# Optimization experiments

Measured on AMD Instinct MI355X. Metric: run time of the kernel, lower is better.

## Reference

```python
import jax, jax.numpy as jnp
import numpy as np
import math

NUM_HEADS = 12
EMBED_DIM = 768

def setup_inputs() -> dict:
    key = jax.random.key(0)
    ks = jax.random.split(key, 9)
    B, T, D = 2, 2048, EMBED_DIM
    s = 1.0 / math.sqrt(D)
    inp = {
        "x": jax.random.normal(ks[0], (B, T, D), dtype=jnp.float32),
        "Wq": jax.random.normal(ks[1], (D, D), dtype=jnp.float32) * s,
        "bq": jnp.zeros((D,), dtype=jnp.float32),
        "Wk": jax.random.normal(ks[2], (D, D), dtype=jnp.float32) * s,
        "bk": jnp.zeros((D,), dtype=jnp.float32),
        "Wv": jax.random.normal(ks[3], (D, D), dtype=jnp.float32) * s,
        "bv": jnp.zeros((D,), dtype=jnp.float32),
        "Wo": jax.random.normal(ks[4], (D, D), dtype=jnp.float32) * s,
        "bo": jnp.zeros((D,), dtype=jnp.float32),
    }
    return inp

def reference(x, Wq, bq, Wk, bk, Wv, bv, Wo, bo):
    B, T, D = x.shape
    H = NUM_HEADS
    Dh = D // H
    # QKV projections, split heads: [B, H, T, Dh]
    def proj(W, b):
        y = x @ W.T + b
        return y.reshape(B, T, H, Dh).transpose(0, 2, 1, 3)
    q = proj(Wq, bq)
    k = proj(Wk, bk)
    v = proj(Wv, bv)
    scores = jnp.einsum('bhtd,bhsd->bhts', q, k) / math.sqrt(Dh)  # [B,H,T,T]
    attn = jax.nn.softmax(scores, axis=-1)
    ctx = jnp.einsum('bhts,bhsd->bhtd', attn, v)  # [B,H,T,Dh]
    ctx = ctx.transpose(0, 2, 1, 3).reshape(B, T, D)
    out = ctx @ Wo.T + bo
    return out
```

## Files before the change

kernel.cpp:

```cpp
#include <hip/hip_runtime.h>
#include <math.h>

using f32x4   = __attribute__((ext_vector_type(4))) float;
using bf16x8  = __attribute__((ext_vector_type(8))) short;

constexpr int Bb = 2;
constexpr int T  = 2048;
constexpr int D  = 768;
constexpr int H  = 12;
constexpr int Dh = 64;
constexpr int M  = Bb * T;
constexpr int NQKV = 3 * D;
#define SCALE_Q 0.18033688011112042f

__device__ __forceinline__ unsigned short f2bf(float f) {
    unsigned u = __float_as_uint(f);
    u += 0x7fffu + ((u >> 16) & 1u);
    return (unsigned short)(u >> 16);
}

__device__ __forceinline__ ushort4 f2bf4(float4 f) {
    return make_ushort4(f2bf(f.x), f2bf(f.y), f2bf(f.z), f2bf(f.w));
}

__device__ __forceinline__ unsigned permpk(float hi_f, float lo_f) {
    return __builtin_amdgcn_perm(__float_as_uint(hi_f), __float_as_uint(lo_f),
                                 0x07060302u);
}

__device__ __forceinline__ void async_copy16(const void* g, void* lds_base) {
    __builtin_amdgcn_global_load_lds(
        (const __attribute__((address_space(1))) unsigned int*)g,
        (__attribute__((address_space(3))) unsigned int*)lds_base, 16, 0, 0);
}

__global__ __launch_bounds__(256) void prep_kernel(
    const float4* __restrict__ x,
    const float4* __restrict__ Wq, const float4* __restrict__ Wk,
    const float4* __restrict__ Wv, const float4* __restrict__ Wo,
    const float* __restrict__ bq, const float* __restrict__ bk, const float* __restrict__ bv,
    ushort4* __restrict__ Xb, ushort4* __restrict__ Wqkvb, ushort4* __restrict__ Wob,
    float* __restrict__ biasS)
{
    const int stride = gridDim.x * 256;
    const int i0 = blockIdx.x * 256 + threadIdx.x;
    const int NX = M * D / 4;
    const int NW = D * D / 4;
    for (int i = i0; i < NX; i += stride) Xb[i] = f2bf4(x[i]);
    for (int i = i0; i < NW; i += stride) {
        Wqkvb[i]          = f2bf4(Wq[i]);
        Wqkvb[NW + i]     = f2bf4(Wk[i]);
        Wqkvb[2 * NW + i] = f2bf4(Wv[i]);
        Wob[i]            = f2bf4(Wo[i]);
    }
    for (int i = i0; i < D; i += stride) {
        biasS[i]         = bq[i];
        biasS[D + i]     = bk[i];
        biasS[2 * D + i] = bv[i];
    }
}

template <int MODE, int TM>
__global__ __launch_bounds__(256) void gemm_bt_kernel(
    const unsigned short* __restrict__ A, const unsigned short* __restrict__ Bm,
    const float* __restrict__ bias, const int Kdim, const int Ndim,
    float* __restrict__ Cout,
    unsigned short* __restrict__ Qo, unsigned short* __restrict__ Ko,
    unsigned short* __restrict__ Vo)
{
    constexpr int IW  = TM / 32;
    constexpr int NCH = (TM + 128) / 8;
    __shared__ unsigned short Sm[(TM + 128) * 64];
    const int tid  = threadIdx.x;
    const int lane = tid & 63, wv = tid >> 6;
    const int l15  = lane & 15, l4 = lane >> 4;
    const int wr   = wv >> 1,  wc = wv & 1;

    const int lin = blockIdx.y * gridDim.x + blockIdx.x;
    const int gx  = (lin >> 3) % gridDim.x;
    const int gy  = (lin / (8 * gridDim.x)) * 8 + (lin & 7);
    const int row0 = gy * TM, col0 = gx * 128;

    f32x4 acc[IW][4];
    #pragma unroll
    for (int i = 0; i < IW; ++i)
        #pragma unroll
        for (int j = 0; j < 4; ++j)
            acc[i][j] = (f32x4){0.f, 0.f, 0.f, 0.f};

    for (int k0 = 0; k0 < Kdim; k0 += 64) {
        __syncthreads();
        #pragma unroll
        for (int ch0 = 0; ch0 < NCH; ch0 += 4) {
            const int ch = ch0 + wv;
            const int offb = ch * 1024;
            const int off  = offb + lane * 16;
            const int r  = off >> 7;
            const int bl = (off & 127) >> 4;
            const int gc = (bl ^ (r & 7)) << 3;
            const unsigned short* src = (r < TM)
                ? A  + (size_t)(row0 + r) * Kdim + k0 + gc
                : Bm + (size_t)(col0 + (r - TM)) * Kdim + k0 + gc;
            async_copy16(src, (char*)Sm + offb);
        }
        __syncthreads();

        #pragma unroll
        for (int c = 0; c < 2; ++c) {
            bf16x8 af[IW], bfr[4];
            #pragma unroll
            for (int i = 0; i < IW; ++i) {
                const int row = wr * (TM / 2) + i * 16 + l15;
                af[i] = *(const bf16x8*)((const char*)Sm +
                        row * 128 + (((c << 2) + l4) ^ (row & 7)) * 16);
            }
            #pragma unroll
            for (int j = 0; j < 4; ++j) {
                const int row = TM + wc * 64 + j * 16 + l15;
                bfr[j] = *(const bf16x8*)((const char*)Sm +
                        row * 128 + (((c << 2) + l4) ^ (row & 7)) * 16);
            }
            #pragma unroll
            for (int i = 0; i < IW; ++i)
                #pragma unroll
                for (int j = 0; j < 4; ++j)
                    acc[i][j] = __builtin_amdgcn_mfma_f32_16x16x32_bf16(af[i], bfr[j], acc[i][j], 0, 0, 0);
        }
    }

    if (MODE == 0) {
        #pragma unroll
        for (int j = 0; j < 4; ++j) {
            const int n = col0 + wc * 64 + j * 16 + l15;
            const float bv_ = bias[n];
            #pragma unroll
            for (int i = 0; i < IW; ++i) {
                #pragma unroll
                for (int r = 0; r < 4; ++r) {
                    const int m = row0 + wr * (TM / 2) + i * 16 + l4 * 4 + r;
                    Cout[(size_t)m * Ndim + n] = acc[i][j][r] + bv_;
                }
            }
        }
    } else {
        #pragma unroll
        for (int j = 0; j < 4; ++j) {
            const int n = col0 + wc * 64 + j * 16 + l15;
            const int which = n / D;
            const int hd = n % D;
            const int h = hd >> 6, d = hd & 63;
            const float bv_ = bias[n];
            if (which == 2) {
                #pragma unroll
                for (int i = 0; i < IW; ++i) {
                    const int m0 = row0 + wr * (TM / 2) + i * 16 + l4 * 4;
                    const int b = m0 >> 11, t = m0 & (T - 1);
                    const int g = (t >> 2) & 3, h16 = (t >> 4) & 1;
                    const int tp = (t & ~31) | (g << 3) | (h16 << 2);
                    float4 v4;
                    v4.x = acc[i][j][0] + bv_; v4.y = acc[i][j][1] + bv_;
                    v4.z = acc[i][j][2] + bv_; v4.w = acc[i][j][3] + bv_;
                    *(ushort4*)&Vo[((size_t)(b * H + h) * Dh + d) * T + tp] = f2bf4(v4);
                }
            } else {
                const float scale = (which == 0) ? SCALE_Q : 1.0f;
                unsigned short* dst = (which == 0) ? Qo : Ko;
                #pragma unroll
                for (int i = 0; i < IW; ++i) {
                    #pragma unroll
                    for (int r = 0; r < 4; ++r) {
                        const int m = row0 + wr * (TM / 2) + i * 16 + l4 * 4 + r;
                        const int b = m >> 11, t = m & (T - 1);
                        dst[((size_t)(b * H + h) * T + t) * Dh + d] =
                            f2bf((acc[i][j][r] + bv_) * scale);
                    }
                }
            }
        }
    }
}

__global__ __launch_bounds__(256) void attn_kernel(
    const unsigned short* __restrict__ Q, const unsigned short* __restrict__ Kg,
    const unsigned short* __restrict__ Vt, unsigned short* __restrict__ Ctx)
{
    __shared__ unsigned short Ks[2][64 * 64];
    __shared__ unsigned short Vs[2][64 * 64];
    const int bh = blockIdx.y;
    const int q0 = blockIdx.x * 128;
    const int tid = threadIdx.x, lane = tid & 63, wv = tid >> 6;
    const int l15 = lane & 15, l4 = lane >> 4;
    const unsigned short* Qp = Q  + (size_t)bh * T * Dh;
    const unsigned short* Kp = Kg + (size_t)bh * T * Dh;
    const unsigned short* Vp = Vt + (size_t)bh * Dh * T;

    bf16x8 qf[2][2];
    #pragma unroll
    for (int qg = 0; qg < 2; ++qg)
        #pragma unroll
        for (int c = 0; c < 2; ++c)
            qf[qg][c] = *(const bf16x8*)&Qp[(size_t)(q0 + wv * 32 + qg * 16 + l15) * Dh + c * 32 + l4 * 8];

    const short oneb = (short)0x3F80;
    const bf16x8 onesf = {oneb, oneb, oneb, oneb, oneb, oneb, oneb, oneb};

    auto load_tiles = [&](int kt, int buf) {
        #pragma unroll
        for (int i = 0; i < 2; ++i) {
            const int offb = wv * 2048 + i * 1024;
            const int off  = offb + lane * 16;
            const int r = off >> 7;
            const int blk = (off & 127) >> 4;
            const int gc = (blk ^ (r & 7)) << 3;
            async_copy16(Kp + (size_t)(kt + r) * Dh + gc, (char*)&Ks[buf][0] + offb);
            async_copy16(Vp + (size_t)r * T + kt + gc,    (char*)&Vs[buf][0] + offb);
        }
    };

    load_tiles(0, 0);
    f32x4 o[2][4], oL[2];
    #pragma unroll
    for (int qg = 0; qg < 2; ++qg) {
        #pragma unroll
        for (int nj = 0; nj < 4; ++nj) o[qg][nj] = (f32x4){0.f, 0.f, 0.f, 0.f};
        oL[qg] = (f32x4){0.f, 0.f, 0.f, 0.f};
    }

    for (int kt64 = 0; kt64 < T / 64; ++kt64) {
        const int cur = kt64 & 1;
        __syncthreads();
        if (kt64 + 1 < T / 64) load_tiles((kt64 + 1) * 64, cur ^ 1);

        const char* Kb = (const char*)&Ks[cur][0];
        const char* Vb = (const char*)&Vs[cur][0];

        f32x4 Sa[2][2];
        #pragma unroll
        for (int t = 0; t < 2; ++t)
            #pragma unroll
            for (int qg = 0; qg < 2; ++qg)
                Sa[t][qg] = (f32x4){0.f, 0.f, 0.f, 0.f};
        #pragma unroll
        for (int c = 0; c < 2; ++c) {
            #pragma unroll
            for (int t = 0; t < 2; ++t) {
                const int row = t * 16 + l15;
                bf16x8 kb = *(const bf16x8*)(Kb + row * 128 + (((c << 2) + l4) ^ (row & 7)) * 16);
                #pragma unroll
                for (int qg = 0; qg < 2; ++qg)
                    Sa[t][qg] = __builtin_amdgcn_mfma_f32_16x16x32_bf16(kb, qf[qg][c], Sa[t][qg], 0, 0, 0);
            }
        }
        #pragma unroll
        for (int t = 0; t < 2; ++t)
            #pragma unroll
            for (int qg = 0; qg < 2; ++qg)
                #pragma unroll
                for (int r = 0; r < 4; ++r)
                    Sa[t][qg][r] = __builtin_amdgcn_exp2f(Sa[t][qg][r]);
        union { unsigned u[4]; bf16x8 v; } p0[2];
        #pragma unroll
        for (int qg = 0; qg < 2; ++qg) {
            p0[qg].u[0] = permpk(Sa[0][qg][1], Sa[0][qg][0]);
            p0[qg].u[1] = permpk(Sa[0][qg][3], Sa[0][qg][2]);
            p0[qg].u[2] = permpk(Sa[1][qg][1], Sa[1][qg][0]);
            p0[qg].u[3] = permpk(Sa[1][qg][3], Sa[1][qg][2]);
        }

        f32x4 Sb[2][2];
        #pragma unroll
        for (int t = 0; t < 2; ++t)
            #pragma unroll
            for (int qg = 0; qg < 2; ++qg)
                Sb[t][qg] = (f32x4){0.f, 0.f, 0.f, 0.f};
        #pragma unroll
        for (int c = 0; c < 2; ++c) {
            #pragma unroll
            for (int t = 0; t < 2; ++t) {
                const int row = (t + 2) * 16 + l15;
                bf16x8 kb = *(const bf16x8*)(Kb + row * 128 + (((c << 2) + l4) ^ (row & 7)) * 16);
                #pragma unroll
                for (int qg = 0; qg < 2; ++qg)
                    Sb[t][qg] = __builtin_amdgcn_mfma_f32_16x16x32_bf16(kb, qf[qg][c], Sb[t][qg], 0, 0, 0);
            }
        }

        #pragma unroll
        for (int qg = 0; qg < 2; ++qg)
            oL[qg] = __builtin_amdgcn_mfma_f32_16x16x32_bf16(p0[qg].v, onesf, oL[qg], 0, 0, 0);
        #pragma unroll
        for (int nj = 0; nj < 4; ++nj) {
            const int row = nj * 16 + l15;
            bf16x8 vb = *(const bf16x8*)(Vb + row * 128 + ((l4) ^ (row & 7)) * 16);
            #pragma unroll
            for (int qg = 0; qg < 2; ++qg)
                o[qg][nj] = __builtin_amdgcn_mfma_f32_16x16x32_bf16(p0[qg].v, vb, o[qg][nj], 0, 0, 0);
        }

        #pragma unroll
        for (int t = 0; t < 2; ++t)
            #pragma unroll
            for (int qg = 0; qg < 2; ++qg)
                #pragma unroll
                for (int r = 0; r < 4; ++r)
                    Sb[t][qg][r] = __builtin_amdgcn_exp2f(Sb[t][qg][r]);
        union { unsigned u[4]; bf16x8 v; } p1[2];
        #pragma unroll
        for (int qg = 0; qg < 2; ++qg) {
            p1[qg].u[0] = permpk(Sb[0][qg][1], Sb[0][qg][0]);
            p1[qg].u[1] = permpk(Sb[0][qg][3], Sb[0][qg][2]);
            p1[qg].u[2] = permpk(Sb[1][qg][1], Sb[1][qg][0]);
            p1[qg].u[3] = permpk(Sb[1][qg][3], Sb[1][qg][2]);
        }

        #pragma unroll
        for (int qg = 0; qg < 2; ++qg)
            oL[qg] = __builtin_amdgcn_mfma_f32_16x16x32_bf16(p1[qg].v, onesf, oL[qg], 0, 0, 0);
        #pragma unroll
        for (int nj = 0; nj < 4; ++nj) {
            const int row = nj * 16 + l15;
            bf16x8 vb = *(const bf16x8*)(Vb + row * 128 + ((4 + l4) ^ (row & 7)) * 16);
            #pragma unroll
            for (int qg = 0; qg < 2; ++qg)
                o[qg][nj] = __builtin_amdgcn_mfma_f32_16x16x32_bf16(p1[qg].v, vb, o[qg][nj], 0, 0, 0);
        }
    }

    const int b = bh / H, h = bh % H;
    #pragma unroll
    for (int qg = 0; qg < 2; ++qg) {
        #pragma unroll
        for (int r = 0; r < 4; ++r) {
            const float inv = 1.0f / oL[qg][r];
            const int t = q0 + wv * 32 + qg * 16 + l4 * 4 + r;
            #pragma unroll
            for (int nj = 0; nj < 4; ++nj) {
                const int col = h * 64 + nj * 16 + l15;
                Ctx[(size_t)(b * T + t) * D + col] = f2bf(o[qg][nj][r] * inv);
            }
        }
    }
}

extern "C" void kernel_launch(void* const* d_in, const int* in_sizes, int n_in,
                              void* d_out, int out_size, void* d_ws, size_t ws_size,
                              hipStream_t stream) {
    const float* x  = (const float*)d_in[0];
    const float* Wq = (const float*)d_in[1];
    const float* bq = (const float*)d_in[2];
    const float* Wk = (const float*)d_in[3];
    const float* bk = (const float*)d_in[4];
    const float* Wv = (const float*)d_in[5];
    const float* bv = (const float*)d_in[6];
    const float* Wo = (const float*)d_in[7];
    const float* bo = (const float*)d_in[8];
    float* out = (float*)d_out;

    char* w = (char*)d_ws;
    auto alloc = [&](size_t bytes) {
        char* p = w; w += (bytes + 255) & ~(size_t)255; return p;
    };
    unsigned short* Xb    = (unsigned short*)alloc((size_t)M * D * 2);
    unsigned short* Wqkvb = (unsigned short*)alloc((size_t)NQKV * D * 2);
    unsigned short* Wob   = (unsigned short*)alloc((size_t)D * D * 2);
    float*          biasS = (float*)alloc((size_t)NQKV * 4);
    unsigned short* Qb    = (unsigned short*)alloc((size_t)M * D * 2);
    unsigned short* Kb    = (unsigned short*)alloc((size_t)M * D * 2);
    unsigned short* Vtb   = (unsigned short*)alloc((size_t)M * D * 2);
    unsigned short* Ctxb  = (unsigned short*)alloc((size_t)M * D * 2);

    prep_kernel<<<1024, 256, 0, stream>>>(
        (const float4*)x, (const float4*)Wq, (const float4*)Wk, (const float4*)Wv,
        (const float4*)Wo, bq, bk, bv,
        (ushort4*)Xb, (ushort4*)Wqkvb, (ushort4*)Wob, biasS);

    gemm_bt_kernel<1, 128><<<dim3(NQKV / 128, M / 128), 256, 0, stream>>>(
        Xb, Wqkvb, biasS, D, NQKV, nullptr, Qb, Kb, Vtb);

    attn_kernel<<<dim3(T / 128, Bb * H), 256, 0, stream>>>(Qb, Kb, Vtb, Ctxb);

    gemm_bt_kernel<0, 64><<<dim3(D / 128, M / 64), 256, 0, stream>>>(
        Ctxb, Wob, bo, D, D, out, nullptr, nullptr, nullptr);
}
```

Before: 168.5 us.

## Split attention KV range across two blocks and double-buffer output-projection GEMM

The attention kernel now processes only half of the key/value sequence per block, with a new grid z-dimension selecting the half. It writes unnormalized fp32 partial outputs and row sums, and a new combine kernel adds the halves, normalizes, and writes bf16 context. The intent is to double the attention grid so the blocks spread more evenly across compute units. The out-projection GEMM gains an optional double-buffered LDS pipeline and uses a smaller 32-row tile, and the prep kernel launches more blocks. The cost is extra global traffic for the fp32 partials plus one more kernel launch. Summing the halves is only correct because the softmax uses no per-block running max.

```diff
diff --git a/kernel.cpp b/kernel.cpp
--- a/kernel.cpp
+++ b/kernel.cpp
@@ -11,6 +11,7 @@
 constexpr int Dh = 64;
 constexpr int M  = Bb * T;
 constexpr int NQKV = 3 * D;
+constexpr int NBH = Bb * H;
 #define SCALE_Q 0.18033688011112042f
 
 __device__ __forceinline__ unsigned short f2bf(float f) {
@@ -60,7 +61,7 @@
     }
 }
 
-template <int MODE, int TM>
+template <int MODE, int TM, int DB>
 __global__ __launch_bounds__(256) void gemm_bt_kernel(
     const unsigned short* __restrict__ A, const unsigned short* __restrict__ Bm,
     const float* __restrict__ bias, const int Kdim, const int Ndim,
@@ -70,7 +71,8 @@
 {
     constexpr int IW  = TM / 32;
     constexpr int NCH = (TM + 128) / 8;
-    __shared__ unsigned short Sm[(TM + 128) * 64];
+    constexpr int TB  = (TM + 128) * 128;
+    __shared__ unsigned short Sm[(TM + 128) * 64 * (DB ? 2 : 1)];
     const int tid  = threadIdx.x;
     const int lane = tid & 63, wv = tid >> 6;
     const int l15  = lane & 15, l4 = lane >> 4;
@@ -81,15 +83,7 @@
     const int gy  = (lin / (8 * gridDim.x)) * 8 + (lin & 7);
     const int row0 = gy * TM, col0 = gx * 128;
 
-    f32x4 acc[IW][4];
-    #pragma unroll
-    for (int i = 0; i < IW; ++i)
-        #pragma unroll
-        for (int j = 0; j < 4; ++j)
-            acc[i][j] = (f32x4){0.f, 0.f, 0.f, 0.f};
-
-    for (int k0 = 0; k0 < Kdim; k0 += 64) {
-        __syncthreads();
+    auto stage = [&](int k0, int b) {
         #pragma unroll
         for (int ch0 = 0; ch0 < NCH; ch0 += 4) {
             const int ch = ch0 + wv;
@@ -101,9 +95,29 @@
             const unsigned short* src = (r < TM)
                 ? A  + (size_t)(row0 + r) * Kdim + k0 + gc
                 : Bm + (size_t)(col0 + (r - TM)) * Kdim + k0 + gc;
-            async_copy16(src, (char*)Sm + offb);
-        }
+            async_copy16(src, (char*)Sm + b * TB + offb);
+        }
+    };
+
+    f32x4 acc[IW][4];
+    #pragma unroll
+    for (int i = 0; i < IW; ++i)
+        #pragma unroll
+        for (int j = 0; j < 4; ++j)
+            acc[i][j] = (f32x4){0.f, 0.f, 0.f, 0.f};
+
+    if (DB) stage(0, 0);
+
+    for (int k0 = 0, it = 0; k0 < Kdim; k0 += 64, ++it) {
+        const int cur = DB ? (it & 1) : 0;
         __syncthreads();
+        if (DB) {
+            if (k0 + 64 < Kdim) stage(k0 + 64, cur ^ 1);
+        } else {
+            stage(k0, 0);
+            __syncthreads();
+        }
+        const char* Sb_ = (const char*)Sm + cur * TB;
 
         #pragma unroll
         for (int c = 0; c < 2; ++c) {
@@ -111,13 +125,13 @@
             #pragma unroll
             for (int i = 0; i < IW; ++i) {
                 const int row = wr * (TM / 2) + i * 16 + l15;
-                af[i] = *(const bf16x8*)((const char*)Sm +
+                af[i] = *(const bf16x8*)(Sb_ +
                         row * 128 + (((c << 2) + l4) ^ (row & 7)) * 16);
             }
             #pragma unroll
             for (int j = 0; j < 4; ++j) {
                 const int row = TM + wc * 64 + j * 16 + l15;
-                bfr[j] = *(const bf16x8*)((const char*)Sm +
+                bfr[j] = *(const bf16x8*)(Sb_ +
                         row * 128 + (((c << 2) + l4) ^ (row & 7)) * 16);
             }
             #pragma unroll
@@ -182,11 +196,13 @@
 
 __global__ __launch_bounds__(256) void attn_kernel(
     const unsigned short* __restrict__ Q, const unsigned short* __restrict__ Kg,
-    const unsigned short* __restrict__ Vt, unsigned short* __restrict__ Ctx)
+    const unsigned short* __restrict__ Vt,
+    float* __restrict__ Po, float* __restrict__ PoL)
 {
     __shared__ unsigned short Ks[2][64 * 64];
     __shared__ unsigned short Vs[2][64 * 64];
     const int bh = blockIdx.y;
+    const int half = blockIdx.z;
     const int q0 = blockIdx.x * 128;
     const int tid = threadIdx.x, lane = tid & 63, wv = tid >> 6;
     const int l15 = lane & 15, l4 = lane >> 4;
@@ -217,7 +233,9 @@
         }
     };
 
-    load_tiles(0, 0);
+    const int NT = T / 128;
+    const int kt0 = half * NT;
+    load_tiles(kt0 * 64, 0);
     f32x4 o[2][4], oL[2];
     #pragma unroll
     for (int qg = 0; qg < 2; ++qg) {
@@ -226,10 +244,11 @@
         oL[qg] = (f32x4){0.f, 0.f, 0.f, 0.f};
     }
 
-    for (int kt64 = 0; kt64 < T / 64; ++kt64) {
-        const int cur = kt64 & 1;
+    for (int it = 0; it < NT; ++it) {
+        const int kt64 = kt0 + it;
+        const int cur = it & 1;
         __syncthreads();
-        if (kt64 + 1 < T / 64) load_tiles((kt64 + 1) * 64, cur ^ 1);
+        if (it + 1 < NT) load_tiles((kt64 + 1) * 64, cur ^ 1);
 
         const char* Kb = (const char*)&Ks[cur][0];
         const char* Vb = (const char*)&Vs[cur][0];
@@ -326,20 +345,36 @@
         }
     }
 
-    const int b = bh / H, h = bh % H;
+    const size_t base = (size_t)(half * NBH + bh) * T;
     #pragma unroll
     for (int qg = 0; qg < 2; ++qg) {
         #pragma unroll
         for (int r = 0; r < 4; ++r) {
-            const float inv = 1.0f / oL[qg][r];
             const int t = q0 + wv * 32 + qg * 16 + l4 * 4 + r;
             #pragma unroll
-            for (int nj = 0; nj < 4; ++nj) {
-                const int col = h * 64 + nj * 16 + l15;
-                Ctx[(size_t)(b * T + t) * D + col] = f2bf(o[qg][nj][r] * inv);
-            }
-        }
-    }
+            for (int nj = 0; nj < 4; ++nj)
+                Po[(base + t) * 64 + nj * 16 + l15] = o[qg][nj][r];
+            if (l15 == 0) PoL[base + t] = oL[qg][r];
+        }
+    }
+}
+
+__global__ __launch_bounds__(256) void combine_kernel(
+    const float4* __restrict__ Po, const float* __restrict__ PoL,
+    unsigned short* __restrict__ Ctx)
+{
+    const int idx = blockIdx.x * 256 + threadIdx.x;
+    const int d4 = idx & 15;
+    const int rem = idx >> 4;
+    const int t = rem & (T - 1), bh = rem >> 11;
+    const float4 a = Po[(size_t)rem * 16 + d4];
+    const float4 c = Po[(size_t)NBH * T * 16 + (size_t)rem * 16 + d4];
+    const float inv = 1.0f / (PoL[rem] + PoL[NBH * T + rem]);
+    const int b = bh / H, h = bh % H;
+    float4 v;
+    v.x = (a.x + c.x) * inv; v.y = (a.y + c.y) * inv;
+    v.z = (a.z + c.z) * inv; v.w = (a.w + c.w) * inv;
+    *(ushort4*)&Ctx[(size_t)(b * T + t) * D + h * 64 + d4 * 4] = f2bf4(v);
 }
 
 extern "C" void kernel_launch(void* const* d_in, const int* in_sizes, int n_in,
@@ -368,17 +403,22 @@
     unsigned short* Kb    = (unsigned short*)alloc((size_t)M * D * 2);
     unsigned short* Vtb   = (unsigned short*)alloc((size_t)M * D * 2);
     unsigned short* Ctxb  = (unsigned short*)alloc((size_t)M * D * 2);
-
-    prep_kernel<<<1024, 256, 0, stream>>>(
+    float*          Po    = (float*)alloc((size_t)2 * NBH * T * 64 * 4);
+    float*          PoL   = (float*)alloc((size_t)2 * NBH * T * 4);
+
+    prep_kernel<<<2048, 256, 0, stream>>>(
         (const float4*)x, (const float4*)Wq, (const float4*)Wk, (const float4*)Wv,
         (const float4*)Wo, bq, bk, bv,
         (ushort4*)Xb, (ushort4*)Wqkvb, (ushort4*)Wob, biasS);
 
-    gemm_bt_kernel<1, 128><<<dim3(NQKV / 128, M / 128), 256, 0, stream>>>(
+    gemm_bt_kernel<1, 128, 0><<<dim3(NQKV / 128, M / 128), 256, 0, stream>>>(
         Xb, Wqkvb, biasS, D, NQKV, nullptr, Qb, Kb, Vtb);
 
-    attn_kernel<<<dim3(T / 128, Bb * H), 256, 0, stream>>>(Qb, Kb, Vtb, Ctxb);
-
-    gemm_bt_kernel<0, 64><<<dim3(D / 128, M / 64), 256, 0, stream>>>(
+    attn_kernel<<<dim3(T / 128, NBH, 2), 256, 0, stream>>>(Qb, Kb, Vtb, Po, PoL);
+
+    combine_kernel<<<NBH * T * 16 / 256, 256, 0, stream>>>(
+        (const float4*)Po, PoL, Ctxb);
+
+    gemm_bt_kernel<0, 32, 1><<<dim3(D / 128, M / 32), 256, 0, stream>>>(
         Ctxb, Wob, bo, D, D, out, nullptr, nullptr, nullptr);
 }
```

New measurement: 160.9 us. -4.5%, faster.
